# Performance work log

Measured on AMD Instinct MI355X. Metric: run time of the kernel, lower is better.

The kernel has to match this reference:

```python
import jax, jax.numpy as jnp
import numpy as np

N_NODES = 100000
N_EDGES = 3200000
F_IN, F_HID, N_ACT = 128, 16, 32


def setup_inputs() -> dict:
    key = jax.random.key(0)
    k1, k2, k3, k4, k5, k6 = jax.random.split(key, 6)
    return {
        "x": jax.random.normal(k1, (N_NODES, F_IN), dtype=jnp.float32),
        "W1": jax.random.normal(k2, (F_IN, F_HID), dtype=jnp.float32) * 0.1,
        "b1": jax.random.normal(k3, (F_HID,), dtype=jnp.float32) * 0.1,
        "W2": jax.random.normal(k4, (F_HID, N_ACT), dtype=jnp.float32) * 0.1,
        "b2": jax.random.normal(k5, (N_ACT,), dtype=jnp.float32) * 0.1,
        "edge_index": jax.random.randint(k6, (2, N_EDGES), 0, N_NODES, dtype=jnp.int64),
    }


def _gcn_layer(h, W, b, src, dst, norm, n):
    # PyG GCNConv: linear first, then normalized scatter-add aggregation, then bias
    h = h @ W                                   # [N, out]
    msg = h[src] * norm[:, None]                # gather + edge scale, [E+N, out]
    agg = jax.ops.segment_sum(msg, dst, num_segments=n)
    return agg + b


def reference(x, W1, b1, W2, b2, edge_index):
    n = x.shape[0]
    loops = jnp.arange(n, dtype=edge_index.dtype)
    src = jnp.concatenate([edge_index[0], loops])  # add self-loops (GCNConv default)
    dst = jnp.concatenate([edge_index[1], loops])
    # symmetric normalization: deg on A + I, norm_e = d_src^-1/2 * d_dst^-1/2
    deg = jax.ops.segment_sum(jnp.ones_like(dst, dtype=x.dtype), dst, num_segments=n)
    dis = jnp.where(deg > 0, jax.lax.rsqrt(deg), 0.0)
    norm = dis[src] * dis[dst]
    h = jax.nn.relu(_gcn_layer(x, W1, b1, src, dst, norm, n))
    return _gcn_layer(h, W2, b2, src, dst, norm, n)
```

## Files before the change

### kernel.cpp

```cpp
#include <hip/hip_runtime.h>
#include <hip/hip_fp16.h>


#define NNODES 100000
#define FIN    128
#define FHID   16
#define NACT   32
#define BUCK   196
#define NB     511
#define MAGIC  21913099u
#define TILE2  8192
#define CAP    8192
#define ASTRIDE 17
#define SCALE    262144.0f
#define INVSCALE 3.814697265625e-06f

__device__ __forceinline__ int bucket_of(int d) {
    return (int)__umulhi((unsigned)d, MAGIC);
}

__device__ __forceinline__ unsigned pack2(float a, float b) {
    __half2 h = __floats2half2_rn(a, b);
    return *reinterpret_cast<unsigned*>(&h);
}

__device__ __forceinline__ float2 h2f(unsigned u) {
    return __half22float2(*reinterpret_cast<__half2*>(&u));
}

__device__ __forceinline__ int wave_iscan(int v, int lane) {
#pragma unroll
    for (int d = 1; d < 64; d <<= 1) {
        int u = __shfl_up(v, d, 64);
        if (lane >= d) v += u;
    }
    return v;
}

__global__ void __launch_bounds__(1024) k_bin(
        const int* __restrict__ src, const int* __restrict__ dst, int E,
        int* __restrict__ gcur, unsigned* __restrict__ binned) {
    __shared__ unsigned staged[TILE2];
    __shared__ int gscat[TILE2];
    __shared__ int hist[NB];
    __shared__ int lcur[NB];
    __shared__ int dbase[NB];
    __shared__ int wsum[16];
    int t = threadIdx.x, lane = t & 63, wv = t >> 6;
    int tb = blockIdx.x * TILE2;
    int tn = min(TILE2, E - tb);

    for (int i = t; i < NB; i += 1024) hist[i] = 0;
    __syncthreads();

    if ((E & 3) == 0) {
        const int4* d4 = (const int4*)(dst + tb);
        int tn4 = tn >> 2;
        for (int i = t; i < tn4; i += 1024) {
            int4 v = d4[i];
            atomicAdd(&hist[bucket_of(v.x)], 1);
            atomicAdd(&hist[bucket_of(v.y)], 1);
            atomicAdd(&hist[bucket_of(v.z)], 1);
            atomicAdd(&hist[bucket_of(v.w)], 1);
        }
        for (int i = (tn4 << 2) + t; i < tn; i += 1024)
            atomicAdd(&hist[bucket_of(dst[tb + i])], 1);
    } else {
        for (int i = t; i < tn; i += 1024)
            atomicAdd(&hist[bucket_of(dst[tb + i])], 1);
    }
    __syncthreads();

    int c = (t < NB) ? hist[t] : 0;
    int incl = wave_iscan(c, lane);
    if (lane == 63) wsum[wv] = incl;
    __syncthreads();
    int add = 0;
#pragma unroll
    for (int i = 0; i < 16; ++i) add += (i < wv) ? wsum[i] : 0;
    incl += add;
    int excl = incl - c;
    if (t < NB) {
        lcur[t] = excl;
        int gb = (c > 0) ? atomicAdd(&gcur[t], c) : 0;
        dbase[t] = t * CAP + gb - excl;
    }
    __syncthreads();

    if ((E & 3) == 0) {
        const int4* d4 = (const int4*)(dst + tb);
        const int4* s4 = (const int4*)(src + tb);
        int tn4 = tn >> 2;
        for (int i = t; i < tn4; i += 1024) {
            int4 dv = d4[i], sv = s4[i];
#pragma unroll
            for (int j = 0; j < 4; ++j) {
                int d = (j == 0) ? dv.x : (j == 1) ? dv.y : (j == 2) ? dv.z : dv.w;
                int s = (j == 0) ? sv.x : (j == 1) ? sv.y : (j == 2) ? sv.z : sv.w;
                int b = bucket_of(d);
                int pos = atomicAdd(&lcur[b], 1);
                staged[pos] = ((unsigned)s << 8) | (unsigned)(d - b * BUCK);
                gscat[pos] = dbase[b] + pos;
            }
        }
        for (int i = (tn4 << 2) + t; i < tn; i += 1024) {
            int d = dst[tb + i], s = src[tb + i];
            int b = bucket_of(d);
            int pos = atomicAdd(&lcur[b], 1);
            staged[pos] = ((unsigned)s << 8) | (unsigned)(d - b * BUCK);
            gscat[pos] = dbase[b] + pos;
        }
    } else {
        for (int i = t; i < tn; i += 1024) {
            int d = dst[tb + i], s = src[tb + i];
            int b = bucket_of(d);
            int pos = atomicAdd(&lcur[b], 1);
            staged[pos] = ((unsigned)s << 8) | (unsigned)(d - b * BUCK);
            gscat[pos] = dbase[b] + pos;
        }
    }
    __syncthreads();
    for (int j = t; j < tn; j += 1024) binned[gscat[j]] = staged[j];
}

#define FMA4(A, S, W) { (A).x += (S) * (W).x; (A).y += (S) * (W).y; \
                        (A).z += (S) * (W).z; (A).w += (S) * (W).w; }

__global__ void __launch_bounds__(256) k_deg_xw1(
        const int* __restrict__ gcur, const unsigned* __restrict__ binned,
        const float* __restrict__ x, const float* __restrict__ W1,
        float* __restrict__ dis, __half* __restrict__ featp, int n) {
    __shared__ int cnt[BUCK];
    __shared__ float sdis[BUCK];
    int t = threadIdx.x;
    int bk = blockIdx.x;
    if (t < BUCK) cnt[t] = 0;
    __syncthreads();
    int beg = bk * CAP, end = beg + gcur[bk];
    for (int i = beg + t; i < end; i += 256) atomicAdd(&cnt[binned[i] & 255], 1);
    __syncthreads();
    int node = bk * BUCK + t;
    if (t < BUCK) {
        float dv = rsqrtf((float)cnt[t] + 1.0f);
        sdis[t] = dv;
        if (node < n) dis[node] = dv;
    }
    __syncthreads();
    if (t >= BUCK || node >= n) return;

    const float4* xr = (const float4*)(x + (size_t)node * FIN);
    const float4* w4 = (const float4*)W1;
    float4 a0 = make_float4(0.f, 0.f, 0.f, 0.f), a1 = a0, a2 = a0, a3 = a0;
#pragma unroll 8
    for (int k4 = 0; k4 < FIN / 4; ++k4) {
        float4 xv = xr[k4];
        int kb = k4 * 16;
        FMA4(a0, xv.x, w4[kb + 0]);  FMA4(a1, xv.x, w4[kb + 1]);
        FMA4(a2, xv.x, w4[kb + 2]);  FMA4(a3, xv.x, w4[kb + 3]);
        FMA4(a0, xv.y, w4[kb + 4]);  FMA4(a1, xv.y, w4[kb + 5]);
        FMA4(a2, xv.y, w4[kb + 6]);  FMA4(a3, xv.y, w4[kb + 7]);
        FMA4(a0, xv.z, w4[kb + 8]);  FMA4(a1, xv.z, w4[kb + 9]);
        FMA4(a2, xv.z, w4[kb + 10]); FMA4(a3, xv.z, w4[kb + 11]);
        FMA4(a0, xv.w, w4[kb + 12]); FMA4(a1, xv.w, w4[kb + 13]);
        FMA4(a2, xv.w, w4[kb + 14]); FMA4(a3, xv.w, w4[kb + 15]);
    }
    float d = sdis[t];
    uint4 w0, w1;
    w0.x = pack2(a0.x * d, a0.y * d); w0.y = pack2(a0.z * d, a0.w * d);
    w0.z = pack2(a1.x * d, a1.y * d); w0.w = pack2(a1.z * d, a1.w * d);
    w1.x = pack2(a2.x * d, a2.y * d); w1.y = pack2(a2.z * d, a2.w * d);
    w1.z = pack2(a3.x * d, a3.y * d); w1.w = pack2(a3.z * d, a3.w * d);
    uint4* hr = (uint4*)(featp + (size_t)node * FHID);
    hr[0] = w0; hr[1] = w1;
}

#define ADD8(U, dptr) { \
    float2 f0_ = h2f((U).x), f1_ = h2f((U).y), f2_ = h2f((U).z), f3_ = h2f((U).w); \
    atomicAdd(&(dptr)[0], __float2int_rn(f0_.x * SCALE)); \
    atomicAdd(&(dptr)[1], __float2int_rn(f0_.y * SCALE)); \
    atomicAdd(&(dptr)[2], __float2int_rn(f1_.x * SCALE)); \
    atomicAdd(&(dptr)[3], __float2int_rn(f1_.y * SCALE)); \
    atomicAdd(&(dptr)[4], __float2int_rn(f2_.x * SCALE)); \
    atomicAdd(&(dptr)[5], __float2int_rn(f2_.y * SCALE)); \
    atomicAdd(&(dptr)[6], __float2int_rn(f3_.x * SCALE)); \
    atomicAdd(&(dptr)[7], __float2int_rn(f3_.y * SCALE)); }

template <int L>
__global__ void __launch_bounds__(1024) k_agg(
        const int* __restrict__ gcur, const unsigned* __restrict__ binned,
        const float* __restrict__ dis, const __half* __restrict__ featp,
        const float* __restrict__ W2, const float* __restrict__ bias,
        void* __restrict__ outp, int n) {
    __shared__ int acc[BUCK * ASTRIDE];
    __shared__ float wb[FHID * NACT];
    __shared__ float bs[NACT];
    int t = threadIdx.x;
    int bk = blockIdx.x;
    int base = bk * BUCK;
    int nn = min(BUCK, n - base);
    const uint4* fp4 = (const uint4*)featp;
    if (L == 2) {
        for (int i = t; i < FHID * NACT; i += 1024) wb[i] = W2[i];
        if (t < NACT) bs[t] = bias[t];
    }
    for (int idx = t; idx < BUCK * 2; idx += 1024) {
        int d = idx >> 1, p2 = idx & 1;
        int* a = &acc[d * ASTRIDE + p2 * 8];
        if (d < nn) {
            uint4 u = fp4[(size_t)((base + d) << 1) + p2];
            float2 f0 = h2f(u.x), f1 = h2f(u.y), f2 = h2f(u.z), f3 = h2f(u.w);
            a[0] = __float2int_rn(f0.x * SCALE);
            a[1] = __float2int_rn(f0.y * SCALE);
            a[2] = __float2int_rn(f1.x * SCALE);
            a[3] = __float2int_rn(f1.y * SCALE);
            a[4] = __float2int_rn(f2.x * SCALE);
            a[5] = __float2int_rn(f2.y * SCALE);
            a[6] = __float2int_rn(f3.x * SCALE);
            a[7] = __float2int_rn(f3.y * SCALE);
        } else {
            a[0] = 0; a[1] = 0; a[2] = 0; a[3] = 0;
            a[4] = 0; a[5] = 0; a[6] = 0; a[7] = 0;
        }
    }
    __syncthreads();
    int beg = bk * CAP, end = beg + gcur[bk];
    int pr = t >> 1, p2 = t & 1;
    int i = beg + pr;
    for (; i + 1536 < end; i += 2048) {
        unsigned e0 = binned[i];
        unsigned e1 = binned[i + 512];
        unsigned e2 = binned[i + 1024];
        unsigned e3 = binned[i + 1536];
        uint4 u0 = fp4[(size_t)((e0 >> 8) << 1) + p2];
        uint4 u1 = fp4[(size_t)((e1 >> 8) << 1) + p2];
        uint4 u2 = fp4[(size_t)((e2 >> 8) << 1) + p2];
        uint4 u3 = fp4[(size_t)((e3 >> 8) << 1) + p2];
        int* d0 = &acc[(int)(e0 & 255) * ASTRIDE + p2 * 8];
        ADD8(u0, d0);
        int* d1 = &acc[(int)(e1 & 255) * ASTRIDE + p2 * 8];
        ADD8(u1, d1);
        int* d2 = &acc[(int)(e2 & 255) * ASTRIDE + p2 * 8];
        ADD8(u2, d2);
        int* d3 = &acc[(int)(e3 & 255) * ASTRIDE + p2 * 8];
        ADD8(u3, d3);
    }
    for (; i < end; i += 512) {
        unsigned e0 = binned[i];
        uint4 u0 = fp4[(size_t)((e0 >> 8) << 1) + p2];
        int* d0 = &acc[(int)(e0 & 255) * ASTRIDE + p2 * 8];
        ADD8(u0, d0);
    }
    __syncthreads();
    if (L == 1) {
        for (int idx = t; idx < nn * 4; idx += 1024) {
            int d = idx >> 2, pp = idx & 3;
            int node = base + d;
            float di = dis[node];
            const int* a = &acc[d * ASTRIDE + pp * 4];
            float4 bv = ((const float4*)bias)[pp];
            float f0 = (float)a[0] * INVSCALE;
            float f1 = (float)a[1] * INVSCALE;
            float f2 = (float)a[2] * INVSCALE;
            float f3 = (float)a[3] * INVSCALE;
            float rx = fmaxf(di * f0 + bv.x, 0.f) * di;
            float ry = fmaxf(di * f1 + bv.y, 0.f) * di;
            float rz = fmaxf(di * f2 + bv.z, 0.f) * di;
            float rw = fmaxf(di * f3 + bv.w, 0.f) * di;
            uint2 w;
            w.x = pack2(rx, ry);
            w.y = pack2(rz, rw);
            ((uint2*)outp)[(size_t)node * 4 + pp] = w;
        }
    } else {
        for (int idx = t; idx < nn * 2; idx += 1024) {
            int d = idx >> 1, h = idx & 1;
            int node = base + d;
            float di = dis[node];
            float p16[FHID];
#pragma unroll
            for (int c = 0; c < FHID; ++c)
                p16[c] = di * ((float)acc[d * ASTRIDE + c] * INVSCALE);
            float o[16];
#pragma unroll
            for (int j = 0; j < 16; ++j) {
                int col = h * 16 + j;
                float s = bs[col];
#pragma unroll
                for (int c = 0; c < FHID; ++c) s += p16[c] * wb[c * NACT + col];
                o[j] = s;
            }
            float4* orow = (float4*)outp + (size_t)node * 8 + h * 4;
            orow[0] = make_float4(o[0], o[1], o[2], o[3]);
            orow[1] = make_float4(o[4], o[5], o[6], o[7]);
            orow[2] = make_float4(o[8], o[9], o[10], o[11]);
            orow[3] = make_float4(o[12], o[13], o[14], o[15]);
        }
    }
}

extern "C" void kernel_launch(void* const* d_in, const int* in_sizes, int n_in,
                              void* d_out, int out_size, void* d_ws, size_t ws_size,
                              hipStream_t stream) {
    const float* x  = (const float*)d_in[0];
    const float* W1 = (const float*)d_in[1];
    const float* b1 = (const float*)d_in[2];
    const float* W2 = (const float*)d_in[3];
    const float* b2 = (const float*)d_in[4];
    const int*   ei = (const int*)d_in[5];
    const int E = in_sizes[5] / 2;
    const int n = NNODES;
    const int npad = n + 8;
    const int* src = ei;
    const int* dst = ei + E;
    const int ntb = (E + TILE2 - 1) / TILE2;

    float* fb    = (float*)d_ws;
    float* dis   = fb;
    __half* featp = (__half*)(fb + (size_t)n);
    __half* h1p   = featp + (size_t)16 * npad;
    int*   ib    = (int*)(h1p + (size_t)16 * npad);
    int*   gcur  = ib;
    unsigned* binned = (unsigned*)(ib + NB + 1);

    (void)hipMemsetAsync(gcur, 0, NB * sizeof(int), stream);

    const int B = 256;
    k_bin<<<ntb, 1024, 0, stream>>>(src, dst, E, gcur, binned);
    k_deg_xw1<<<NB, B, 0, stream>>>(gcur, binned, x, W1, dis, featp, n);
    k_agg<1><<<NB, 1024, 0, stream>>>(gcur, binned, dis, featp, nullptr, b1, (void*)h1p, n);
    k_agg<2><<<NB, 1024, 0, stream>>>(gcur, binned, dis, h1p, W2, b2, d_out, n);
}
```

Before: 184.1 us.

## Pack two biased fixed-point accumulators into 64-bit LDS atomics

Scatter-add accumulation in LDS now packs two features into one 64-bit atomic, adding a per-value offset so each 32-bit half stays non-negative and no carry crosses into the upper half. The offset is removed at the end using the stored in-degree plus one. This halves the number of LDS atomic operations per edge. The degree count also switches to uint4 loads of the binned entries. The cost is a per-node degree array and reliance on the biased values never overflowing 32 bits, which limits headroom for high-degree nodes.

```diff
diff --git a/kernel.cpp b/kernel.cpp
--- a/kernel.cpp
+++ b/kernel.cpp
@@ -11,9 +11,11 @@
 #define MAGIC  21913099u
 #define TILE2  8192
 #define CAP    8192
-#define ASTRIDE 17
+#define AST64  9
 #define SCALE    262144.0f
 #define INVSCALE 3.814697265625e-06f
+#define BIASF  4194304.0f
+#define BIASI  4194304u
 
 __device__ __forceinline__ int bucket_of(int d) {
     return (int)__umulhi((unsigned)d, MAGIC);
@@ -26,6 +28,12 @@
 
 __device__ __forceinline__ float2 h2f(unsigned u) {
     return __half22float2(*reinterpret_cast<__half2*>(&u));
+}
+
+__device__ __forceinline__ unsigned long long pk2(float a, float b) {
+    unsigned lo = (unsigned)__float2int_rn(fmaf(a, SCALE, BIASF));
+    unsigned hi = (unsigned)__float2int_rn(fmaf(b, SCALE, BIASF));
+    return (unsigned long long)lo | ((unsigned long long)hi << 32);
 }
 
 __device__ __forceinline__ int wave_iscan(int v, int lane) {
@@ -129,21 +137,32 @@
 __global__ void __launch_bounds__(256) k_deg_xw1(
         const int* __restrict__ gcur, const unsigned* __restrict__ binned,
         const float* __restrict__ x, const float* __restrict__ W1,
-        float* __restrict__ dis, __half* __restrict__ featp, int n) {
+        float* __restrict__ dis, int* __restrict__ deg,
+        __half* __restrict__ featp, int n) {
     __shared__ int cnt[BUCK];
     __shared__ float sdis[BUCK];
     int t = threadIdx.x;
     int bk = blockIdx.x;
     if (t < BUCK) cnt[t] = 0;
     __syncthreads();
-    int beg = bk * CAP, end = beg + gcur[bk];
-    for (int i = beg + t; i < end; i += 256) atomicAdd(&cnt[binned[i] & 255], 1);
+    int beg = bk * CAP, cntE = gcur[bk];
+    const uint4* b4 = (const uint4*)(binned + beg);
+    int n4 = cntE >> 2;
+    for (int i = t; i < n4; i += 256) {
+        uint4 v = b4[i];
+        atomicAdd(&cnt[v.x & 255], 1);
+        atomicAdd(&cnt[v.y & 255], 1);
+        atomicAdd(&cnt[v.z & 255], 1);
+        atomicAdd(&cnt[v.w & 255], 1);
+    }
+    for (int i = (n4 << 2) + t; i < cntE; i += 256)
+        atomicAdd(&cnt[binned[beg + i] & 255], 1);
     __syncthreads();
     int node = bk * BUCK + t;
     if (t < BUCK) {
         float dv = rsqrtf((float)cnt[t] + 1.0f);
         sdis[t] = dv;
-        if (node < n) dis[node] = dv;
+        if (node < n) { dis[node] = dv; deg[node] = cnt[t]; }
     }
     __syncthreads();
     if (t >= BUCK || node >= n) return;
@@ -174,24 +193,21 @@
     hr[0] = w0; hr[1] = w1;
 }
 
-#define ADD8(U, dptr) { \
+#define ADD8P(U, dptr) { \
     float2 f0_ = h2f((U).x), f1_ = h2f((U).y), f2_ = h2f((U).z), f3_ = h2f((U).w); \
-    atomicAdd(&(dptr)[0], __float2int_rn(f0_.x * SCALE)); \
-    atomicAdd(&(dptr)[1], __float2int_rn(f0_.y * SCALE)); \
-    atomicAdd(&(dptr)[2], __float2int_rn(f1_.x * SCALE)); \
-    atomicAdd(&(dptr)[3], __float2int_rn(f1_.y * SCALE)); \
-    atomicAdd(&(dptr)[4], __float2int_rn(f2_.x * SCALE)); \
-    atomicAdd(&(dptr)[5], __float2int_rn(f2_.y * SCALE)); \
-    atomicAdd(&(dptr)[6], __float2int_rn(f3_.x * SCALE)); \
-    atomicAdd(&(dptr)[7], __float2int_rn(f3_.y * SCALE)); }
+    atomicAdd(&(dptr)[0], pk2(f0_.x, f0_.y)); \
+    atomicAdd(&(dptr)[1], pk2(f1_.x, f1_.y)); \
+    atomicAdd(&(dptr)[2], pk2(f2_.x, f2_.y)); \
+    atomicAdd(&(dptr)[3], pk2(f3_.x, f3_.y)); }
 
 template <int L>
 __global__ void __launch_bounds__(1024) k_agg(
         const int* __restrict__ gcur, const unsigned* __restrict__ binned,
-        const float* __restrict__ dis, const __half* __restrict__ featp,
+        const float* __restrict__ dis, const int* __restrict__ deg,
+        const __half* __restrict__ featp,
         const float* __restrict__ W2, const float* __restrict__ bias,
         void* __restrict__ outp, int n) {
-    __shared__ int acc[BUCK * ASTRIDE];
+    __shared__ unsigned long long acc[BUCK * AST64];
     __shared__ float wb[FHID * NACT];
     __shared__ float bs[NACT];
     int t = threadIdx.x;
@@ -205,21 +221,16 @@
     }
     for (int idx = t; idx < BUCK * 2; idx += 1024) {
         int d = idx >> 1, p2 = idx & 1;
-        int* a = &acc[d * ASTRIDE + p2 * 8];
+        unsigned long long* a = &acc[d * AST64 + p2 * 4];
         if (d < nn) {
             uint4 u = fp4[(size_t)((base + d) << 1) + p2];
             float2 f0 = h2f(u.x), f1 = h2f(u.y), f2 = h2f(u.z), f3 = h2f(u.w);
-            a[0] = __float2int_rn(f0.x * SCALE);
-            a[1] = __float2int_rn(f0.y * SCALE);
-            a[2] = __float2int_rn(f1.x * SCALE);
-            a[3] = __float2int_rn(f1.y * SCALE);
-            a[4] = __float2int_rn(f2.x * SCALE);
-            a[5] = __float2int_rn(f2.y * SCALE);
-            a[6] = __float2int_rn(f3.x * SCALE);
-            a[7] = __float2int_rn(f3.y * SCALE);
+            a[0] = pk2(f0.x, f0.y);
+            a[1] = pk2(f1.x, f1.y);
+            a[2] = pk2(f2.x, f2.y);
+            a[3] = pk2(f3.x, f3.y);
         } else {
-            a[0] = 0; a[1] = 0; a[2] = 0; a[3] = 0;
-            a[4] = 0; a[5] = 0; a[6] = 0; a[7] = 0;
+            a[0] = 0ull; a[1] = 0ull; a[2] = 0ull; a[3] = 0ull;
         }
     }
     __syncthreads();
@@ -235,20 +246,20 @@
         uint4 u1 = fp4[(size_t)((e1 >> 8) << 1) + p2];
         uint4 u2 = fp4[(size_t)((e2 >> 8) << 1) + p2];
         uint4 u3 = fp4[(size_t)((e3 >> 8) << 1) + p2];
-        int* d0 = &acc[(int)(e0 & 255) * ASTRIDE + p2 * 8];
-        ADD8(u0, d0);
-        int* d1 = &acc[(int)(e1 & 255) * ASTRIDE + p2 * 8];
-        ADD8(u1, d1);
-        int* d2 = &acc[(int)(e2 & 255) * ASTRIDE + p2 * 8];
-        ADD8(u2, d2);
-        int* d3 = &acc[(int)(e3 & 255) * ASTRIDE + p2 * 8];
-        ADD8(u3, d3);
+        unsigned long long* d0 = &acc[(int)(e0 & 255) * AST64 + p2 * 4];
+        ADD8P(u0, d0);
+        unsigned long long* d1 = &acc[(int)(e1 & 255) * AST64 + p2 * 4];
+        ADD8P(u1, d1);
+        unsigned long long* d2 = &acc[(int)(e2 & 255) * AST64 + p2 * 4];
+        ADD8P(u2, d2);
+        unsigned long long* d3 = &acc[(int)(e3 & 255) * AST64 + p2 * 4];
+        ADD8P(u3, d3);
     }
     for (; i < end; i += 512) {
         unsigned e0 = binned[i];
         uint4 u0 = fp4[(size_t)((e0 >> 8) << 1) + p2];
-        int* d0 = &acc[(int)(e0 & 255) * ASTRIDE + p2 * 8];
-        ADD8(u0, d0);
+        unsigned long long* d0 = &acc[(int)(e0 & 255) * AST64 + p2 * 4];
+        ADD8P(u0, d0);
     }
     __syncthreads();
     if (L == 1) {
@@ -256,12 +267,14 @@
             int d = idx >> 2, pp = idx & 3;
             int node = base + d;
             float di = dis[node];
-            const int* a = &acc[d * ASTRIDE + pp * 4];
+            unsigned bb = (unsigned)(deg[node] + 1) * BIASI;
+            const unsigned long long* a = &acc[d * AST64 + pp * 2];
+            unsigned long long w0 = a[0], w1 = a[1];
+            float f0 = (float)(int)((unsigned)w0 - bb) * INVSCALE;
+            float f1 = (float)(int)((unsigned)(w0 >> 32) - bb) * INVSCALE;
+            float f2 = (float)(int)((unsigned)w1 - bb) * INVSCALE;
+            float f3 = (float)(int)((unsigned)(w1 >> 32) - bb) * INVSCALE;
             float4 bv = ((const float4*)bias)[pp];
-            float f0 = (float)a[0] * INVSCALE;
-            float f1 = (float)a[1] * INVSCALE;
-            float f2 = (float)a[2] * INVSCALE;
-            float f3 = (float)a[3] * INVSCALE;
             float rx = fmaxf(di * f0 + bv.x, 0.f) * di;
             float ry = fmaxf(di * f1 + bv.y, 0.f) * di;
             float rz = fmaxf(di * f2 + bv.z, 0.f) * di;
@@ -276,10 +289,14 @@
             int d = idx >> 1, h = idx & 1;
             int node = base + d;
             float di = dis[node];
+            unsigned bb = (unsigned)(deg[node] + 1) * BIASI;
             float p16[FHID];
 #pragma unroll
-            for (int c = 0; c < FHID; ++c)
-                p16[c] = di * ((float)acc[d * ASTRIDE + c] * INVSCALE);
+            for (int c = 0; c < 8; ++c) {
+                unsigned long long w = acc[d * AST64 + c];
+                p16[2 * c]     = di * ((float)(int)((unsigned)w - bb) * INVSCALE);
+                p16[2 * c + 1] = di * ((float)(int)((unsigned)(w >> 32) - bb) * INVSCALE);
+            }
             float o[16];
 #pragma unroll
             for (int j = 0; j < 16; ++j) {
@@ -320,13 +337,14 @@
     __half* h1p   = featp + (size_t)16 * npad;
     int*   ib    = (int*)(h1p + (size_t)16 * npad);
     int*   gcur  = ib;
-    unsigned* binned = (unsigned*)(ib + NB + 1);
+    int*   deg   = ib + NB + 1;
+    unsigned* binned = (unsigned*)(deg + n);
 
     (void)hipMemsetAsync(gcur, 0, NB * sizeof(int), stream);
 
     const int B = 256;
     k_bin<<<ntb, 1024, 0, stream>>>(src, dst, E, gcur, binned);
-    k_deg_xw1<<<NB, B, 0, stream>>>(gcur, binned, x, W1, dis, featp, n);
-    k_agg<1><<<NB, 1024, 0, stream>>>(gcur, binned, dis, featp, nullptr, b1, (void*)h1p, n);
-    k_agg<2><<<NB, 1024, 0, stream>>>(gcur, binned, dis, h1p, W2, b2, d_out, n);
-}
+    k_deg_xw1<<<NB, B, 0, stream>>>(gcur, binned, x, W1, dis, deg, featp, n);
+    k_agg<1><<<NB, 1024, 0, stream>>>(gcur, binned, dis, deg, featp, nullptr, b1, (void*)h1p, n);
+    k_agg<2><<<NB, 1024, 0, stream>>>(gcur, binned, dis, deg, h1p, W2, b2, d_out, n);
+}
```

New measurement: 182.1 us. Within noise of the previous version (-1.1%).
